# Kernel tuning notes

Measured on AMD Instinct MI355X. Metric: run time of the kernel, lower is better.

The kernel has to match this reference:

```python
import jax, jax.numpy as jnp
import numpy as np

N = 100000
E = 1600000
IN_DIM = 128
HID = 64
HEADS = 4
OUT_DIM = 64
NEG_SLOPE = 0.2


def _xavier(key, shape):
    fan_in, fan_out = shape[0], shape[1]
    limit = float(np.sqrt(6.0 / (fan_in + fan_out)))
    return jax.random.uniform(key, shape, jnp.float32, -limit, limit)


def setup_inputs() -> dict:
    key = jax.random.key(0)
    ks = jax.random.split(key, 8)
    x = jax.random.normal(ks[0], (N, IN_DIM), jnp.float32)
    edge_index = jax.random.randint(ks[1], (2, E), 0, N, dtype=jnp.int32)
    # Layer 0: in=128 -> heads=4, out=64, concat
    W0 = _xavier(ks[2], (IN_DIM, HEADS * HID))
    a0 = _xavier(ks[3], (HEADS, 2 * HID))
    # Layer 1: in=256 -> heads=4, out=64, concat
    W1 = _xavier(ks[4], (HEADS * HID, HEADS * HID))
    a1 = _xavier(ks[5], (HEADS, 2 * HID))
    # Layer 2 (output): in=256 -> heads=1, out=64, no concat
    W2 = _xavier(ks[6], (HEADS * HID, 1 * OUT_DIM))
    a2 = _xavier(ks[7], (1, 2 * OUT_DIM))
    return {"x": x, "edge_index": edge_index,
            "W0": W0, "a0": a0, "W1": W1, "a1": a1, "W2": W2, "a2": a2}


def gat_layer(x, src, dst, W, a, heads, out_dim, concat):
    n = x.shape[0]
    h = (x @ W).reshape(n, heads, out_dim)            # [N, H, D]
    a_s, a_d = a[:, :out_dim], a[:, out_dim:]          # [H, D] each
    alpha_s = jnp.einsum('nhd,hd->nh', h, a_s)         # [N, H]
    alpha_d = jnp.einsum('nhd,hd->nh', h, a_d)         # [N, H]
    e = jax.nn.leaky_relu(alpha_s[src] + alpha_d[dst], NEG_SLOPE)  # [E, H]
    # segment softmax over edges grouped by destination node
    e_max = jax.lax.stop_gradient(jax.ops.segment_max(e, dst, num_segments=n))
    e_max = jnp.where(jnp.isfinite(e_max), e_max, 0.0)
    e_exp = jnp.exp(e - e_max[dst])                    # [E, H]
    denom = jax.ops.segment_sum(e_exp, dst, num_segments=n)  # [N, H]
    att = e_exp / (denom[dst] + 1e-16)                 # [E, H]
    msg = h[src] * att[:, :, None]                     # [E, H, D]
    out = jax.ops.segment_sum(msg, dst, num_segments=n)  # [N, H, D]
    if concat:
        return out.reshape(n, heads * out_dim)
    return out.mean(axis=1)


def reference(x, edge_index, W0, a0, W1, a1, W2, a2):
    src, dst = edge_index[0], edge_index[1]
    # layer 0 + ELU (dropout is identity in eval mode)
    h = gat_layer(x, src, dst, W0, a0, HEADS, HID, True)
    h = jax.nn.elu(h)
    # layer 1 + ELU
    h = gat_layer(h, src, dst, W1, a1, HEADS, HID, True)
    h = jax.nn.elu(h)
    # output layer: single head, no concat, no activation
    out = gat_layer(h, src, dst, W2, a2, 1, OUT_DIM, False)
    return out
```

## Files before the change

### kernel.cpp

```cpp
#include <hip/hip_runtime.h>
#include <math.h>

#define NEG_SLOPE 0.2f

typedef short short8 __attribute__((ext_vector_type(8)));
typedef float float4v __attribute__((ext_vector_type(4)));
typedef _Float16 h8 __attribute__((ext_vector_type(8)));

__device__ __forceinline__ unsigned short f2bf(float f) {
    unsigned u = __float_as_uint(f);
    unsigned r = (u + 0x7fff + ((u >> 16) & 1)) >> 16;
    return (unsigned short)r;
}
__device__ __forceinline__ float bf2f(unsigned short h) {
    return __uint_as_float(((unsigned)h) << 16);
}
__device__ __forceinline__ unsigned short f2h(float f) {
    _Float16 t = (_Float16)f;
    return *(unsigned short*)&t;
}

__device__ __forceinline__ void gload_lds16(const void* g, void* l) {
    __builtin_amdgcn_global_load_lds(
        (const __attribute__((address_space(1))) unsigned int*)g,
        (__attribute__((address_space(3))) unsigned int*)l, 16, 0, 0);
}


__global__ void count_kernel(const int* __restrict__ dst, int E, int* __restrict__ counts) {
    int i = blockIdx.x * blockDim.x + threadIdx.x;
    if (i < E) atomicAdd(&counts[dst[i]], 1);
}

__global__ void scan1_kernel(const int* __restrict__ in, int n, int* __restrict__ bsums) {
    __shared__ int sdata[256];
    int tid = threadIdx.x;
    int base = blockIdx.x * 1024 + tid * 4;
    int s = 0;
#pragma unroll
    for (int j = 0; j < 4; ++j) if (base + j < n) s += in[base + j];
    sdata[tid] = s; __syncthreads();
    for (int off = 128; off > 0; off >>= 1) {
        if (tid < off) sdata[tid] += sdata[tid + off];
        __syncthreads();
    }
    if (tid == 0) bsums[blockIdx.x] = sdata[0];
}

__global__ void scan2_kernel(int* bsums, int nb) {
    __shared__ int sd[128];
    int tid = threadIdx.x;
    int v = (tid < nb) ? bsums[tid] : 0;
    sd[tid] = v; __syncthreads();
    for (int off = 1; off < 128; off <<= 1) {
        int t = (tid >= off) ? sd[tid - off] : 0;
        __syncthreads();
        sd[tid] += t;
        __syncthreads();
    }
    if (tid < nb) bsums[tid] = sd[tid] - v;
}

__global__ void scan3_kernel(const int* __restrict__ in, int n, const int* __restrict__ bsums,
                             int* __restrict__ row_ptr, int* __restrict__ cursor, int E) {
    __shared__ int sdata[256];
    int tid = threadIdx.x;
    int base = blockIdx.x * 1024 + tid * 4;
    int v[4]; int s = 0;
#pragma unroll
    for (int j = 0; j < 4; ++j) { v[j] = (base + j < n) ? in[base + j] : 0; s += v[j]; }
    sdata[tid] = s; __syncthreads();
    for (int off = 1; off < 256; off <<= 1) {
        int t = (tid >= off) ? sdata[tid - off] : 0;
        __syncthreads();
        sdata[tid] += t;
        __syncthreads();
    }
    int excl = sdata[tid] - s;
    int run = bsums[blockIdx.x] + excl;
#pragma unroll
    for (int j = 0; j < 4; ++j) {
        if (base + j < n) { row_ptr[base + j] = run; cursor[base + j] = run; run += v[j]; }
    }
    if (blockIdx.x == 0 && tid == 0) row_ptr[n] = E;
}

__global__ void fill_kernel(const int* __restrict__ dst, const int* __restrict__ src, int E,
                            int* __restrict__ cursor, int* __restrict__ sperm) {
    int i = blockIdx.x * blockDim.x + threadIdx.x;
    if (i < E) {
        int p = atomicAdd(&cursor[dst[i]], 1);
        sperm[p] = src[i];
    }
}


__global__ __launch_bounds__(256) void prep_kernel(
    const float* __restrict__ W0, const float* __restrict__ W1, const float* __restrict__ W2,
    const float* __restrict__ a0, const float* __restrict__ a1, const float* __restrict__ a2,
    unsigned short* __restrict__ WT0, unsigned short* __restrict__ WT1, unsigned short* __restrict__ WT2,
    unsigned short* __restrict__ wa0, unsigned short* __restrict__ wa1, unsigned short* __restrict__ wa2) {
    int i = blockIdx.x * 256 + threadIdx.x;
    if (i < 32768) {
        int k = i >> 8, n = i & 255;
        WT0[n * 128 + k] = f2bf(W0[i]);
    } else if (i < 98304) {
        int j = i - 32768;
        int k = j >> 8, n = j & 255;
        WT1[n * 256 + k] = f2bf(W1[j]);
    } else if (i < 114688) {
        int j = i - 98304;
        int k = j >> 6, n = j & 63;
        WT2[n * 256 + k] = f2bf(W2[j]);
    } else if (i < 114688 + 2048) {
        int t = i - 114688;
        int k = t >> 4, j8 = t & 15;
        float s = 0.f;
        if (j8 < 8) {
            int h = j8 & 3, off = (j8 >> 2) * 64;
            for (int d = 0; d < 64; ++d)
                s += W0[k * 256 + h * 64 + d] * a0[h * 128 + off + d];
        }
        wa0[j8 * 128 + k] = f2bf(s);
    } else if (i < 114688 + 2048 + 4096) {
        int t = i - 114688 - 2048;
        int k = t >> 4, j8 = t & 15;
        float s = 0.f;
        if (j8 < 8) {
            int h = j8 & 3, off = (j8 >> 2) * 64;
            for (int d = 0; d < 64; ++d)
                s += W1[k * 256 + h * 64 + d] * a1[h * 128 + off + d];
        }
        wa1[j8 * 256 + k] = f2bf(s);
    } else if (i < 114688 + 2048 + 4096 + 4096) {
        int t = i - 114688 - 2048 - 4096;
        int k = t >> 4, j8 = t & 15;
        float s = 0.f;
        if (j8 < 2) {
            for (int d = 0; d < 64; ++d)
                s += W2[k * 64 + d] * a2[j8 * 64 + d];
        }
        wa2[j8 * 256 + k] = f2bf(s);
    }
}

__global__ void xcvt_kernel(const float* __restrict__ X, unsigned short* __restrict__ b, int total) {
    int i = blockIdx.x * 256 + threadIdx.x;
    if (i >= total) return;
    b[i] = f2bf(X[i]);
}


template <int BN>
__global__ __launch_bounds__(256) void gemm_fused(
    const unsigned short* __restrict__ A, const unsigned short* __restrict__ WT,
    const unsigned short* __restrict__ waSDT,
    unsigned short* __restrict__ hf16,
    float* __restrict__ as_, float* __restrict__ ad_,
    int M, int K) {
    __shared__ unsigned short AL[128 * 32];
    __shared__ unsigned short BL[BN * 32];
    __shared__ unsigned short WaL[16 * 32];

    int t = threadIdx.x;
    int w = t >> 6, lane = t & 63;
    int q = lane >> 4, i16 = lane & 15;
    int rowBase = blockIdx.x * 128;
    int colBase = blockIdx.y * BN;

    constexpr int MT = (BN == 128) ? 4 : 2;
    int wrow = (BN == 128) ? (w >> 1) * 64 : w * 32;
    int wcol = (BN == 128) ? (w & 1) * 64 : 0;

    bool alphaBlk = (blockIdx.y == 0);
    bool alphaWave = alphaBlk && ((BN == 64) || ((w & 1) == 0));

    float4v acc[MT][4];
    float4v accA[MT];
#pragma unroll
    for (int mt = 0; mt < MT; ++mt) {
        accA[mt] = (float4v)(0.f);
#pragma unroll
        for (int nt = 0; nt < 4; ++nt) acc[mt][nt] = (float4v)(0.f);
    }

    int srow = t >> 2;
    int skq = (t & 3) * 8;

    for (int k0 = 0; k0 < K; k0 += 32) {
        gload_lds16(A + (size_t)(rowBase + srow) * K + k0 + skq, AL + w * 512);
        gload_lds16(A + (size_t)(rowBase + 64 + srow) * K + k0 + skq, AL + 2048 + w * 512);
        gload_lds16(WT + (size_t)(colBase + srow) * K + k0 + skq, BL + w * 512);
        if (BN == 128)
            gload_lds16(WT + (size_t)(colBase + 64 + srow) * K + k0 + skq, BL + 2048 + w * 512);
        if (alphaBlk && w == 0)
            gload_lds16(waSDT + (size_t)srow * K + k0 + skq, WaL);
        __syncthreads();

        short8 af[MT], bf[4];
#pragma unroll
        for (int mt = 0; mt < MT; ++mt)
            af[mt] = *(short8*)&AL[(wrow + mt * 16 + i16) * 32 + q * 8];
#pragma unroll
        for (int nt = 0; nt < 4; ++nt)
            bf[nt] = *(short8*)&BL[(wcol + nt * 16 + i16) * 32 + q * 8];
#pragma unroll
        for (int mt = 0; mt < MT; ++mt)
#pragma unroll
            for (int nt = 0; nt < 4; ++nt)
                acc[mt][nt] = __builtin_amdgcn_mfma_f32_16x16x32_bf16(af[mt], bf[nt], acc[mt][nt], 0, 0, 0);
        if (alphaWave) {
            short8 aw = *(short8*)&WaL[i16 * 32 + q * 8];
#pragma unroll
            for (int mt = 0; mt < MT; ++mt)
                accA[mt] = __builtin_amdgcn_mfma_f32_16x16x32_bf16(af[mt], aw, accA[mt], 0, 0, 0);
        }
        __syncthreads();
    }

    int cb0 = colBase + wcol;
#pragma unroll
    for (int mt = 0; mt < MT; ++mt)
#pragma unroll
        for (int r = 0; r < 4; ++r) {
            int grow = rowBase + wrow + mt * 16 + q * 4 + r;
            bool ok = grow < M;
            if (ok) {
#pragma unroll
                for (int nt = 0; nt < 4; ++nt) {
                    float v = acc[mt][nt][r];
                    if (BN == 128) hf16[(size_t)grow * 256 + cb0 + nt * 16 + i16] = f2h(v);
                    else           hf16[(size_t)grow * 64 + nt * 16 + i16] = f2h(v);
                }
                if (alphaWave) {
                    float av = accA[mt][r];
                    if (BN == 128) {
                        if (i16 < 4)      as_[grow * 4 + i16] = av;
                        else if (i16 < 8) ad_[grow * 4 + (i16 - 4)] = av;
                    } else {
                        if (i16 == 0)      as_[grow] = av;
                        else if (i16 == 1) ad_[grow] = av;
                    }
                }
            }
        }
}


__global__ __launch_bounds__(256) void aggregate4(
    const unsigned short* __restrict__ hf16, const int* __restrict__ row_ptr,
    const int* __restrict__ sperm, const float* __restrict__ as_, const float* __restrict__ ad_,
    unsigned short* __restrict__ outB, int n) {
    int w = threadIdx.x >> 6, lane = threadIdx.x & 63;
    int node = blockIdx.x * 4 + w;
    if (node >= n) return;
    int beg = row_ptr[node], end = row_ptr[node + 1];
    int deg = end - beg;
    int myh = lane & 3;
    float ad_my = ad_[node * 4 + myh];

    int half = lane >> 5;
    int dg = lane & 31;
    int hh = dg >> 3;
    float acc[8];
#pragma unroll
    for (int k = 0; k < 8; ++k) acc[k] = 0.f;
    float lsum = 0.f;

    const char* hbase = (const char*)hf16;
    unsigned dgo = (unsigned)dg << 4;

    for (int el0 = 0; el0 < deg; el0 += 16) {
        int ne = deg - el0; if (ne > 16) ne = 16;
        int eSlot = lane >> 2;
        float att = 0.f; int sMy = 0;
        if (eSlot < ne) {
            sMy = sperm[beg + el0 + eSlot];
            float e = as_[sMy * 4 + myh] + ad_my;
            e = e > 0.f ? e : NEG_SLOPE * e;
            att = __expf(e);
        }
        lsum += att;

        int j = 0;
        for (; j + 8 <= ne; j += 8) {
            int sl0 = j + half, sl1 = j + 2 + half, sl2 = j + 4 + half, sl3 = j + 6 + half;
            float a0 = __shfl(att, sl0 * 4 + hh, 64);
            int   s0 = __shfl(sMy, sl0 * 4, 64);
            float a1 = __shfl(att, sl1 * 4 + hh, 64);
            int   s1 = __shfl(sMy, sl1 * 4, 64);
            float a2 = __shfl(att, sl2 * 4 + hh, 64);
            int   s2 = __shfl(sMy, sl2 * 4, 64);
            float a3 = __shfl(att, sl3 * 4 + hh, 64);
            int   s3 = __shfl(sMy, sl3 * 4, 64);
            h8 v0 = *(const h8*)(hbase + (((unsigned)s0 << 9) + dgo));
            h8 v1 = *(const h8*)(hbase + (((unsigned)s1 << 9) + dgo));
            h8 v2 = *(const h8*)(hbase + (((unsigned)s2 << 9) + dgo));
            h8 v3 = *(const h8*)(hbase + (((unsigned)s3 << 9) + dgo));
#pragma unroll
            for (int k = 0; k < 8; ++k) acc[k] += a0 * (float)v0[k];
#pragma unroll
            for (int k = 0; k < 8; ++k) acc[k] += a1 * (float)v1[k];
#pragma unroll
            for (int k = 0; k < 8; ++k) acc[k] += a2 * (float)v2[k];
#pragma unroll
            for (int k = 0; k < 8; ++k) acc[k] += a3 * (float)v3[k];
        }
        for (; j < ne; j += 2) {
            int sl = j + half;
            float a = __shfl(att, sl * 4 + hh, 64);
            int   s = __shfl(sMy, sl * 4, 64);
            h8 v = *(const h8*)(hbase + (((unsigned)s << 9) + dgo));
#pragma unroll
            for (int k = 0; k < 8; ++k) acc[k] += a * (float)v[k];
        }
    }

#pragma unroll
    for (int m = 4; m < 64; m <<= 1) lsum += __shfl_xor(lsum, m, 64);
    float inv = 1.f / (lsum + 1e-16f);
    float invh = __shfl(inv, hh, 64);

#pragma unroll
    for (int k = 0; k < 8; ++k) {
        acc[k] += __shfl_xor(acc[k], 32, 64);
        acc[k] *= invh;
    }

    if (half == 0) {
        short8 hv;
#pragma unroll
        for (int k = 0; k < 8; ++k) {
            float o = acc[k] > 0.f ? acc[k] : expm1f(acc[k]);
            hv[k] = (short)f2bf(o);
        }
        *(short8*)(outB + (size_t)node * 256 + dg * 8) = hv;
    }
}


__global__ __launch_bounds__(256) void aggregate1(
    const unsigned short* __restrict__ hf16, const int* __restrict__ row_ptr,
    const int* __restrict__ sperm, const float* __restrict__ as_, const float* __restrict__ ad_,
    float* __restrict__ out, int n) {
    int w = threadIdx.x >> 6, lane = threadIdx.x & 63;
    int node = blockIdx.x * 4 + w;
    if (node >= n) return;
    int beg = row_ptr[node], end = row_ptr[node + 1];
    int deg = end - beg;
    float ad_n = ad_[node];

    int eg = lane >> 3;
    int dg = lane & 7;
    float acc[8];
#pragma unroll
    for (int k = 0; k < 8; ++k) acc[k] = 0.f;
    float lsum = 0.f;

    const char* hbase = (const char*)hf16;
    unsigned dgo = (unsigned)dg << 4;

    for (int el0 = 0; el0 < deg; el0 += 64) {
        int ne = deg - el0; if (ne > 64) ne = 64;
        float att = 0.f; int sMy = 0;
        if (lane < ne) {
            sMy = sperm[beg + el0 + lane];
            float e = as_[sMy] + ad_n;
            e = e > 0.f ? e : NEG_SLOPE * e;
            att = __expf(e);
        }
        lsum += att;

        int j = 0;
        for (; j + 32 <= ne; j += 32) {
            int sl0 = j + eg, sl1 = j + 8 + eg, sl2 = j + 16 + eg, sl3 = j + 24 + eg;
            float a0 = __shfl(att, sl0, 64);
            int   s0 = __shfl(sMy, sl0, 64);
            float a1 = __shfl(att, sl1, 64);
            int   s1 = __shfl(sMy, sl1, 64);
            float a2 = __shfl(att, sl2, 64);
            int   s2 = __shfl(sMy, sl2, 64);
            float a3 = __shfl(att, sl3, 64);
            int   s3 = __shfl(sMy, sl3, 64);
            h8 v0 = *(const h8*)(hbase + (((unsigned)s0 << 7) + dgo));
            h8 v1 = *(const h8*)(hbase + (((unsigned)s1 << 7) + dgo));
            h8 v2 = *(const h8*)(hbase + (((unsigned)s2 << 7) + dgo));
            h8 v3 = *(const h8*)(hbase + (((unsigned)s3 << 7) + dgo));
#pragma unroll
            for (int k = 0; k < 8; ++k) acc[k] += a0 * (float)v0[k];
#pragma unroll
            for (int k = 0; k < 8; ++k) acc[k] += a1 * (float)v1[k];
#pragma unroll
            for (int k = 0; k < 8; ++k) acc[k] += a2 * (float)v2[k];
#pragma unroll
            for (int k = 0; k < 8; ++k) acc[k] += a3 * (float)v3[k];
        }
        for (; j < ne; j += 8) {
            int sl = j + eg;
            float a = __shfl(att, sl, 64);
            int   s = __shfl(sMy, sl, 64);
            h8 v = *(const h8*)(hbase + (((unsigned)s << 7) + dgo));
#pragma unroll
            for (int k = 0; k < 8; ++k) acc[k] += a * (float)v[k];
        }
    }

#pragma unroll
    for (int m = 1; m < 64; m <<= 1) lsum += __shfl_xor(lsum, m, 64);
    float inv = 1.f / (lsum + 1e-16f);

#pragma unroll
    for (int m = 8; m < 64; m <<= 1)
#pragma unroll
        for (int k = 0; k < 8; ++k) acc[k] += __shfl_xor(acc[k], m, 64);

    if (eg == 0) {
        float4 o0 = make_float4(acc[0] * inv, acc[1] * inv, acc[2] * inv, acc[3] * inv);
        float4 o1 = make_float4(acc[4] * inv, acc[5] * inv, acc[6] * inv, acc[7] * inv);
        *(float4*)(out + (size_t)node * 64 + dg * 8) = o0;
        *(float4*)(out + (size_t)node * 64 + dg * 8 + 4) = o1;
    }
}


extern "C" void kernel_launch(void* const* d_in, const int* in_sizes, int n_in,
                              void* d_out, int out_size, void* d_ws, size_t ws_size,
                              hipStream_t stream) {
    const float* x  = (const float*)d_in[0];
    const int*   ei = (const int*)d_in[1];
    const float* W0 = (const float*)d_in[2];
    const float* a0 = (const float*)d_in[3];
    const float* W1 = (const float*)d_in[4];
    const float* a1 = (const float*)d_in[5];
    const float* W2 = (const float*)d_in[6];
    const float* a2 = (const float*)d_in[7];
    float* out = (float*)d_out;

    int N = in_sizes[0] / 128;
    int E = in_sizes[1] / 2;
    int Npad = (N + 127) & ~127;
    const int* srcp = ei;
    const int* dstp = ei + E;

    char* ws = (char*)d_ws;
    size_t off = 0;
    auto alloc = [&](size_t bytes) -> void* {
        void* p = ws + off;
        off += (bytes + 255) & ~(size_t)255;
        return p;
    };
    unsigned short* xbf  = (unsigned short*)alloc((size_t)Npad * 128 * 2);
    unsigned short* actB = (unsigned short*)alloc((size_t)Npad * 256 * 2);
    unsigned short* hf16 = (unsigned short*)alloc((size_t)Npad * 256 * 2);
    unsigned short* Cf16 = (unsigned short*)alloc((size_t)Npad * 64 * 2);
    float* as_    = (float*)alloc((size_t)N * 4 * 4);
    float* ad_    = (float*)alloc((size_t)N * 4 * 4);
    int*   counts = (int*)alloc((size_t)N * 4);
    int*   row_ptr= (int*)alloc((size_t)(N + 1) * 4);
    int*   cursor = (int*)alloc((size_t)N * 4);
    int*   sperm  = (int*)alloc((size_t)E * 4);
    unsigned short* WT0 = (unsigned short*)alloc((size_t)256 * 128 * 2);
    unsigned short* WT1 = (unsigned short*)alloc((size_t)256 * 256 * 2);
    unsigned short* WT2 = (unsigned short*)alloc((size_t)64 * 256 * 2);
    unsigned short* wa0 = (unsigned short*)alloc((size_t)16 * 128 * 2);
    unsigned short* wa1 = (unsigned short*)alloc((size_t)16 * 256 * 2);
    unsigned short* wa2 = (unsigned short*)alloc((size_t)16 * 256 * 2);
    int*   bsums  = (int*)alloc(4096);

    hipMemsetAsync(counts, 0, (size_t)N * 4, stream);
    int egrid = (E + 255) / 256;
    count_kernel<<<egrid, 256, 0, stream>>>(dstp, E, counts);
    int nb = (N + 1023) / 1024;
    scan1_kernel<<<nb, 256, 0, stream>>>(counts, N, bsums);
    scan2_kernel<<<1, 128, 0, stream>>>(bsums, nb);
    scan3_kernel<<<nb, 256, 0, stream>>>(counts, N, bsums, row_ptr, cursor, E);
    fill_kernel<<<egrid, 256, 0, stream>>>(dstp, srcp, E, cursor, sperm);

    prep_kernel<<<(114688 + 10240 + 255) / 256, 256, 0, stream>>>(
        W0, W1, W2, a0, a1, a2, WT0, WT1, WT2, wa0, wa1, wa2);
    xcvt_kernel<<<((N * 128) + 255) / 256, 256, 0, stream>>>(x, xbf, N * 128);

    int gemm_gx = Npad / 128;
    int ngrid4 = (N + 3) / 4;

    gemm_fused<128><<<dim3(gemm_gx, 2), 256, 0, stream>>>(xbf, WT0, wa0, hf16, as_, ad_, N, 128);
    aggregate4<<<ngrid4, 256, 0, stream>>>(hf16, row_ptr, sperm, as_, ad_, actB, N);

    gemm_fused<128><<<dim3(gemm_gx, 2), 256, 0, stream>>>(actB, WT1, wa1, hf16, as_, ad_, N, 256);
    aggregate4<<<ngrid4, 256, 0, stream>>>(hf16, row_ptr, sperm, as_, ad_, actB, N);

    gemm_fused<64><<<dim3(gemm_gx, 1), 256, 0, stream>>>(actB, WT2, wa2, Cf16, as_, ad_, N, 256);
    aggregate1<<<ngrid4, 256, 0, stream>>>(Cf16, row_ptr, sperm, as_, ad_, out, N);
}
```

Measured before the change: 697.7 us.

## Process two destination nodes per wavefront in GAT aggregation kernels

Each wavefront in both aggregation kernels now handles two consecutive destination nodes, interleaving their edge gathers so twice as many independent loads are in flight per loop iteration. Fixed-size sub-chunks with predicated masking replace the variable tail loops, and the grid is halved. The cost is extra register pressure (two accumulator sets), wasted gather work when the two nodes' degrees differ, and gathers for inactive slots that all hit row 0.

```diff
diff --git a/kernel.cpp b/kernel.cpp
--- a/kernel.cpp
+++ b/kernel.cpp
@@ -252,89 +252,128 @@
     const int* __restrict__ sperm, const float* __restrict__ as_, const float* __restrict__ ad_,
     unsigned short* __restrict__ outB, int n) {
     int w = threadIdx.x >> 6, lane = threadIdx.x & 63;
-    int node = blockIdx.x * 4 + w;
-    if (node >= n) return;
-    int beg = row_ptr[node], end = row_ptr[node + 1];
-    int deg = end - beg;
+    int nodeA = blockIdx.x * 8 + w * 2;
+    if (nodeA >= n) return;
+    int nodeB = nodeA + 1;
+    bool hasB = nodeB < n;
+
+    int begA = row_ptr[nodeA];
+    int degA = row_ptr[nodeA + 1] - begA;
+    int begB = 0, degB = 0;
+    if (hasB) { begB = row_ptr[nodeB]; degB = row_ptr[nodeB + 1] - begB; }
+
     int myh = lane & 3;
-    float ad_my = ad_[node * 4 + myh];
+    float adA = ad_[nodeA * 4 + myh];
+    float adB = hasB ? ad_[nodeB * 4 + myh] : 0.f;
 
     int half = lane >> 5;
     int dg = lane & 31;
     int hh = dg >> 3;
-    float acc[8];
-#pragma unroll
-    for (int k = 0; k < 8; ++k) acc[k] = 0.f;
-    float lsum = 0.f;
+    float accA[8], accB[8];
+#pragma unroll
+    for (int k = 0; k < 8; ++k) { accA[k] = 0.f; accB[k] = 0.f; }
+    float lsumA = 0.f, lsumB = 0.f;
 
     const char* hbase = (const char*)hf16;
     unsigned dgo = (unsigned)dg << 4;
-
-    for (int el0 = 0; el0 < deg; el0 += 16) {
-        int ne = deg - el0; if (ne > 16) ne = 16;
-        int eSlot = lane >> 2;
-        float att = 0.f; int sMy = 0;
-        if (eSlot < ne) {
-            sMy = sperm[beg + el0 + eSlot];
-            float e = as_[sMy * 4 + myh] + ad_my;
+    int eSlot = lane >> 2;
+
+    int degM = degA > degB ? degA : degB;
+    for (int el0 = 0; el0 < degM; el0 += 16) {
+        int neA = degA - el0; if (neA > 16) neA = 16;
+        int neB = degB - el0; if (neB > 16) neB = 16;
+
+        float attA = 0.f; int sAr = 0;
+        if (eSlot < neA) {
+            sAr = sperm[begA + el0 + eSlot];
+            float e = as_[sAr * 4 + myh] + adA;
             e = e > 0.f ? e : NEG_SLOPE * e;
-            att = __expf(e);
-        }
-        lsum += att;
-
-        int j = 0;
-        for (; j + 8 <= ne; j += 8) {
-            int sl0 = j + half, sl1 = j + 2 + half, sl2 = j + 4 + half, sl3 = j + 6 + half;
-            float a0 = __shfl(att, sl0 * 4 + hh, 64);
-            int   s0 = __shfl(sMy, sl0 * 4, 64);
-            float a1 = __shfl(att, sl1 * 4 + hh, 64);
-            int   s1 = __shfl(sMy, sl1 * 4, 64);
-            float a2 = __shfl(att, sl2 * 4 + hh, 64);
-            int   s2 = __shfl(sMy, sl2 * 4, 64);
-            float a3 = __shfl(att, sl3 * 4 + hh, 64);
-            int   s3 = __shfl(sMy, sl3 * 4, 64);
-            h8 v0 = *(const h8*)(hbase + (((unsigned)s0 << 9) + dgo));
-            h8 v1 = *(const h8*)(hbase + (((unsigned)s1 << 9) + dgo));
-            h8 v2 = *(const h8*)(hbase + (((unsigned)s2 << 9) + dgo));
-            h8 v3 = *(const h8*)(hbase + (((unsigned)s3 << 9) + dgo));
-#pragma unroll
-            for (int k = 0; k < 8; ++k) acc[k] += a0 * (float)v0[k];
-#pragma unroll
-            for (int k = 0; k < 8; ++k) acc[k] += a1 * (float)v1[k];
-#pragma unroll
-            for (int k = 0; k < 8; ++k) acc[k] += a2 * (float)v2[k];
-#pragma unroll
-            for (int k = 0; k < 8; ++k) acc[k] += a3 * (float)v3[k];
-        }
-        for (; j < ne; j += 2) {
-            int sl = j + half;
-            float a = __shfl(att, sl * 4 + hh, 64);
-            int   s = __shfl(sMy, sl * 4, 64);
-            h8 v = *(const h8*)(hbase + (((unsigned)s << 9) + dgo));
-#pragma unroll
-            for (int k = 0; k < 8; ++k) acc[k] += a * (float)v[k];
-        }
-    }
-
-#pragma unroll
-    for (int m = 4; m < 64; m <<= 1) lsum += __shfl_xor(lsum, m, 64);
-    float inv = 1.f / (lsum + 1e-16f);
-    float invh = __shfl(inv, hh, 64);
+            attA = __expf(e);
+        }
+        float attB = 0.f; int sBr = 0;
+        if (eSlot < neB) {
+            sBr = sperm[begB + el0 + eSlot];
+            float e = as_[sBr * 4 + myh] + adB;
+            e = e > 0.f ? e : NEG_SLOPE * e;
+            attB = __expf(e);
+        }
+        lsumA += attA; lsumB += attB;
+
+        auto sub8 = [&](int j) {
+            int sl0 = (j + half) * 4, sl1 = (j + 2 + half) * 4,
+                sl2 = (j + 4 + half) * 4, sl3 = (j + 6 + half) * 4;
+            float aA0 = __shfl(attA, sl0 + hh, 64);
+            float aA1 = __shfl(attA, sl1 + hh, 64);
+            float aA2 = __shfl(attA, sl2 + hh, 64);
+            float aA3 = __shfl(attA, sl3 + hh, 64);
+            int   sA0 = __shfl(sAr, sl0, 64);
+            int   sA1 = __shfl(sAr, sl1, 64);
+            int   sA2 = __shfl(sAr, sl2, 64);
+            int   sA3 = __shfl(sAr, sl3, 64);
+            float aB0 = __shfl(attB, sl0 + hh, 64);
+            float aB1 = __shfl(attB, sl1 + hh, 64);
+            float aB2 = __shfl(attB, sl2 + hh, 64);
+            float aB3 = __shfl(attB, sl3 + hh, 64);
+            int   sB0 = __shfl(sBr, sl0, 64);
+            int   sB1 = __shfl(sBr, sl1, 64);
+            int   sB2 = __shfl(sBr, sl2, 64);
+            int   sB3 = __shfl(sBr, sl3, 64);
+            h8 vA0 = *(const h8*)(hbase + (((unsigned)sA0 << 9) + dgo));
+            h8 vA1 = *(const h8*)(hbase + (((unsigned)sA1 << 9) + dgo));
+            h8 vA2 = *(const h8*)(hbase + (((unsigned)sA2 << 9) + dgo));
+            h8 vA3 = *(const h8*)(hbase + (((unsigned)sA3 << 9) + dgo));
+            h8 vB0 = *(const h8*)(hbase + (((unsigned)sB0 << 9) + dgo));
+            h8 vB1 = *(const h8*)(hbase + (((unsigned)sB1 << 9) + dgo));
+            h8 vB2 = *(const h8*)(hbase + (((unsigned)sB2 << 9) + dgo));
+            h8 vB3 = *(const h8*)(hbase + (((unsigned)sB3 << 9) + dgo));
+#pragma unroll
+            for (int k = 0; k < 8; ++k) accA[k] += aA0 * (float)vA0[k];
+#pragma unroll
+            for (int k = 0; k < 8; ++k) accA[k] += aA1 * (float)vA1[k];
+#pragma unroll
+            for (int k = 0; k < 8; ++k) accA[k] += aA2 * (float)vA2[k];
+#pragma unroll
+            for (int k = 0; k < 8; ++k) accA[k] += aA3 * (float)vA3[k];
+#pragma unroll
+            for (int k = 0; k < 8; ++k) accB[k] += aB0 * (float)vB0[k];
+#pragma unroll
+            for (int k = 0; k < 8; ++k) accB[k] += aB1 * (float)vB1[k];
+#pragma unroll
+            for (int k = 0; k < 8; ++k) accB[k] += aB2 * (float)vB2[k];
+#pragma unroll
+            for (int k = 0; k < 8; ++k) accB[k] += aB3 * (float)vB3[k];
+        };
+        sub8(0);
+        if (neA > 8 || neB > 8) sub8(8);
+    }
+
+#pragma unroll
+    for (int m = 4; m < 64; m <<= 1) {
+        lsumA += __shfl_xor(lsumA, m, 64);
+        lsumB += __shfl_xor(lsumB, m, 64);
+    }
+    float invA = 1.f / (lsumA + 1e-16f);
+    float invB = 1.f / (lsumB + 1e-16f);
+    float invhA = __shfl(invA, hh, 64);
+    float invhB = __shfl(invB, hh, 64);
 
 #pragma unroll
     for (int k = 0; k < 8; ++k) {
-        acc[k] += __shfl_xor(acc[k], 32, 64);
-        acc[k] *= invh;
-    }
-
-    if (half == 0) {
+        accA[k] += __shfl_xor(accA[k], 32, 64);
+        accB[k] += __shfl_xor(accB[k], 32, 64);
+    }
+
+    int nodeW = half ? nodeB : nodeA;
+    if (nodeW < n) {
+        float invW = half ? invhB : invhA;
         short8 hv;
 #pragma unroll
         for (int k = 0; k < 8; ++k) {
-            float o = acc[k] > 0.f ? acc[k] : expm1f(acc[k]);
+            float o = (half ? accB[k] : accA[k]) * invW;
+            o = o > 0.f ? o : expm1f(o);
             hv[k] = (short)f2bf(o);
         }
-        *(short8*)(outB + (size_t)node * 256 + dg * 8) = hv;
+        *(short8*)(outB + (size_t)nodeW * 256 + dg * 8) = hv;
     }
 }
 
@@ -344,81 +383,106 @@
     const int* __restrict__ sperm, const float* __restrict__ as_, const float* __restrict__ ad_,
     float* __restrict__ out, int n) {
     int w = threadIdx.x >> 6, lane = threadIdx.x & 63;
-    int node = blockIdx.x * 4 + w;
-    if (node >= n) return;
-    int beg = row_ptr[node], end = row_ptr[node + 1];
-    int deg = end - beg;
-    float ad_n = ad_[node];
+    int nodeA = blockIdx.x * 8 + w * 2;
+    if (nodeA >= n) return;
+    int nodeB = nodeA + 1;
+    bool hasB = nodeB < n;
+
+    int begA = row_ptr[nodeA];
+    int degA = row_ptr[nodeA + 1] - begA;
+    int begB = 0, degB = 0;
+    if (hasB) { begB = row_ptr[nodeB]; degB = row_ptr[nodeB + 1] - begB; }
+    float adA = as_ ? 0.f : 0.f;
+    float adnA = ad_[nodeA];
+    float adnB = hasB ? ad_[nodeB] : 0.f;
+    (void)adA;
 
     int eg = lane >> 3;
     int dg = lane & 7;
-    float acc[8];
-#pragma unroll
-    for (int k = 0; k < 8; ++k) acc[k] = 0.f;
-    float lsum = 0.f;
+    float accA[8], accB[8];
+#pragma unroll
+    for (int k = 0; k < 8; ++k) { accA[k] = 0.f; accB[k] = 0.f; }
+    float lsumA = 0.f, lsumB = 0.f;
 
     const char* hbase = (const char*)hf16;
     unsigned dgo = (unsigned)dg << 4;
 
-    for (int el0 = 0; el0 < deg; el0 += 64) {
-        int ne = deg - el0; if (ne > 64) ne = 64;
-        float att = 0.f; int sMy = 0;
-        if (lane < ne) {
-            sMy = sperm[beg + el0 + lane];
-            float e = as_[sMy] + ad_n;
+    int degM = degA > degB ? degA : degB;
+    for (int el0 = 0; el0 < degM; el0 += 64) {
+        int neA = degA - el0; if (neA > 64) neA = 64;
+        int neB = degB - el0; if (neB > 64) neB = 64;
+
+        float attA = 0.f; int sAr = 0;
+        if (lane < neA) {
+            sAr = sperm[begA + el0 + lane];
+            float e = as_[sAr] + adnA;
             e = e > 0.f ? e : NEG_SLOPE * e;
-            att = __expf(e);
-        }
-        lsum += att;
-
-        int j = 0;
-        for (; j + 32 <= ne; j += 32) {
-            int sl0 = j + eg, sl1 = j + 8 + eg, sl2 = j + 16 + eg, sl3 = j + 24 + eg;
-            float a0 = __shfl(att, sl0, 64);
-            int   s0 = __shfl(sMy, sl0, 64);
-            float a1 = __shfl(att, sl1, 64);
-            int   s1 = __shfl(sMy, sl1, 64);
-            float a2 = __shfl(att, sl2, 64);
-            int   s2 = __shfl(sMy, sl2, 64);
-            float a3 = __shfl(att, sl3, 64);
-            int   s3 = __shfl(sMy, sl3, 64);
-            h8 v0 = *(const h8*)(hbase + (((unsigned)s0 << 7) + dgo));
-            h8 v1 = *(const h8*)(hbase + (((unsigned)s1 << 7) + dgo));
-            h8 v2 = *(const h8*)(hbase + (((unsigned)s2 << 7) + dgo));
-            h8 v3 = *(const h8*)(hbase + (((unsigned)s3 << 7) + dgo));
-#pragma unroll
-            for (int k = 0; k < 8; ++k) acc[k] += a0 * (float)v0[k];
-#pragma unroll
-            for (int k = 0; k < 8; ++k) acc[k] += a1 * (float)v1[k];
-#pragma unroll
-            for (int k = 0; k < 8; ++k) acc[k] += a2 * (float)v2[k];
-#pragma unroll
-            for (int k = 0; k < 8; ++k) acc[k] += a3 * (float)v3[k];
-        }
-        for (; j < ne; j += 8) {
-            int sl = j + eg;
-            float a = __shfl(att, sl, 64);
-            int   s = __shfl(sMy, sl, 64);
-            h8 v = *(const h8*)(hbase + (((unsigned)s << 7) + dgo));
-#pragma unroll
-            for (int k = 0; k < 8; ++k) acc[k] += a * (float)v[k];
-        }
-    }
-
-#pragma unroll
-    for (int m = 1; m < 64; m <<= 1) lsum += __shfl_xor(lsum, m, 64);
-    float inv = 1.f / (lsum + 1e-16f);
+            attA = __expf(e);
+        }
+        float attB = 0.f; int sBr = 0;
+        if (lane < neB) {
+            sBr = sperm[begB + el0 + lane];
+            float e = as_[sBr] + adnB;
+            e = e > 0.f ? e : NEG_SLOPE * e;
+            attB = __expf(e);
+        }
+        lsumA += attA; lsumB += attB;
+
+        auto sub16 = [&](int j) {
+            int sl0 = j + eg, sl1 = j + 8 + eg;
+            float aA0 = __shfl(attA, sl0, 64);
+            float aA1 = __shfl(attA, sl1, 64);
+            int   sA0 = __shfl(sAr, sl0, 64);
+            int   sA1 = __shfl(sAr, sl1, 64);
+            float aB0 = __shfl(attB, sl0, 64);
+            float aB1 = __shfl(attB, sl1, 64);
+            int   sB0 = __shfl(sBr, sl0, 64);
+            int   sB1 = __shfl(sBr, sl1, 64);
+            h8 vA0 = *(const h8*)(hbase + (((unsigned)sA0 << 7) + dgo));
+            h8 vA1 = *(const h8*)(hbase + (((unsigned)sA1 << 7) + dgo));
+            h8 vB0 = *(const h8*)(hbase + (((unsigned)sB0 << 7) + dgo));
+            h8 vB1 = *(const h8*)(hbase + (((unsigned)sB1 << 7) + dgo));
+#pragma unroll
+            for (int k = 0; k < 8; ++k) accA[k] += aA0 * (float)vA0[k];
+#pragma unroll
+            for (int k = 0; k < 8; ++k) accA[k] += aA1 * (float)vA1[k];
+#pragma unroll
+            for (int k = 0; k < 8; ++k) accB[k] += aB0 * (float)vB0[k];
+#pragma unroll
+            for (int k = 0; k < 8; ++k) accB[k] += aB1 * (float)vB1[k];
+        };
+        sub16(0);
+        if (neA > 16 || neB > 16) sub16(16);
+        if (neA > 32 || neB > 32) sub16(32);
+        if (neA > 48 || neB > 48) sub16(48);
+    }
+
+#pragma unroll
+    for (int m = 1; m < 64; m <<= 1) {
+        lsumA += __shfl_xor(lsumA, m, 64);
+        lsumB += __shfl_xor(lsumB, m, 64);
+    }
+    float invA = 1.f / (lsumA + 1e-16f);
+    float invB = 1.f / (lsumB + 1e-16f);
 
 #pragma unroll
     for (int m = 8; m < 64; m <<= 1)
 #pragma unroll
-        for (int k = 0; k < 8; ++k) acc[k] += __shfl_xor(acc[k], m, 64);
+        for (int k = 0; k < 8; ++k) {
+            accA[k] += __shfl_xor(accA[k], m, 64);
+            accB[k] += __shfl_xor(accB[k], m, 64);
+        }
 
     if (eg == 0) {
-        float4 o0 = make_float4(acc[0] * inv, acc[1] * inv, acc[2] * inv, acc[3] * inv);
-        float4 o1 = make_float4(acc[4] * inv, acc[5] * inv, acc[6] * inv, acc[7] * inv);
-        *(float4*)(out + (size_t)node * 64 + dg * 8) = o0;
-        *(float4*)(out + (size_t)node * 64 + dg * 8 + 4) = o1;
+        float4 o0 = make_float4(accA[0] * invA, accA[1] * invA, accA[2] * invA, accA[3] * invA);
+        float4 o1 = make_float4(accA[4] * invA, accA[5] * invA, accA[6] * invA, accA[7] * invA);
+        *(float4*)(out + (size_t)nodeA * 64 + dg * 8) = o0;
+        *(float4*)(out + (size_t)nodeA * 64 + dg * 8 + 4) = o1;
+    } else if (eg == 1 && hasB) {
+        float4 o0 = make_float4(accB[0] * invB, accB[1] * invB, accB[2] * invB, accB[3] * invB);
+        float4 o1 = make_float4(accB[4] * invB, accB[5] * invB, accB[6] * invB, accB[7] * invB);
+        *(float4*)(out + (size_t)nodeB * 64 + dg * 8) = o0;
+        *(float4*)(out + (size_t)nodeB * 64 + dg * 8 + 4) = o1;
     }
 }
 
@@ -481,14 +545,14 @@
     xcvt_kernel<<<((N * 128) + 255) / 256, 256, 0, stream>>>(x, xbf, N * 128);
 
     int gemm_gx = Npad / 128;
-    int ngrid4 = (N + 3) / 4;
+    int ngrid8 = (N + 7) / 8;
 
     gemm_fused<128><<<dim3(gemm_gx, 2), 256, 0, stream>>>(xbf, WT0, wa0, hf16, as_, ad_, N, 128);
-    aggregate4<<<ngrid4, 256, 0, stream>>>(hf16, row_ptr, sperm, as_, ad_, actB, N);
+    aggregate4<<<ngrid8, 256, 0, stream>>>(hf16, row_ptr, sperm, as_, ad_, actB, N);
 
     gemm_fused<128><<<dim3(gemm_gx, 2), 256, 0, stream>>>(actB, WT1, wa1, hf16, as_, ad_, N, 256);
-    aggregate4<<<ngrid4, 256, 0, stream>>>(hf16, row_ptr, sperm, as_, ad_, actB, N);
+    aggregate4<<<ngrid8, 256, 0, stream>>>(hf16, row_ptr, sperm, as_, ad_, actB, N);
 
     gemm_fused<64><<<dim3(gemm_gx, 1), 256, 0, stream>>>(actB, WT2, wa2, Cf16, as_, ad_, N, 256);
-    aggregate1<<<ngrid4, 256, 0, stream>>>(Cf16, row_ptr, sperm, as_, ad_, out, N);
-}
+    aggregate1<<<ngrid8, 256, 0, stream>>>(Cf16, row_ptr, sperm, as_, ad_, out, N);
+}
```

Measured after the change: 709.0 us. No clear change (+1.6%).
